# Optimization experiments

Hardware: AMD Instinct MI355X
Metric: run time of the kernel (lower is better)

Reference implementation:

```python
import jax, jax.numpy as jnp
import numpy as np

DELTA_SCALE = 0.99
DELTA_MIN = 0.01


def setup_inputs() -> dict:
    key = jax.random.key(0)
    ks = jax.random.split(key, 6)
    B, S, Dm, N = 8, 4096, 1024, 16
    x = jax.random.normal(ks[0], (B, S, Dm), dtype=jnp.float32)
    A = jax.random.normal(ks[1], (N,), dtype=jnp.float32) * 0.1 - 1.0
    W_b = jax.random.normal(ks[2], (N, Dm), dtype=jnp.float32) / np.sqrt(Dm)
    b_b = jnp.zeros((N,), dtype=jnp.float32)
    W_c = jax.random.normal(ks[3], (Dm, N), dtype=jnp.float32) / np.sqrt(N)
    b_c = jnp.zeros((Dm,), dtype=jnp.float32)
    D = jnp.ones((Dm,), dtype=jnp.float32)
    W_t = jax.random.normal(ks[4], (1, Dm), dtype=jnp.float32) / np.sqrt(Dm)
    b_t = jnp.zeros((1,), dtype=jnp.float32)
    W_o = jax.random.normal(ks[5], (Dm, Dm), dtype=jnp.float32) / np.sqrt(Dm)
    b_o = jnp.zeros((Dm,), dtype=jnp.float32)
    return {"x": x, "A": A, "W_b": W_b, "b_b": b_b, "W_c": W_c, "b_c": b_c,
            "D": D, "W_t": W_t, "b_t": b_t, "W_o": W_o, "b_o": b_o}


def _scan_combine(left, right):
    # h_t = a_t * h_{t-1} + b_t ; compose two affine maps
    a_l, u_l = left
    a_r, u_r = right
    return (a_l * a_r, a_r * u_l + u_r)


def reference(x, A, W_b, b_b, W_c, b_c, D, W_t, b_t, W_o, b_o):
    # x: [B, S, Dm]
    delta = jax.nn.sigmoid(jnp.einsum('bsd,od->bso', x, W_t) + b_t)  # [B,S,1]
    delta = delta * DELTA_SCALE + DELTA_MIN
    Bu = jnp.einsum('bsd,nd->bsn', x, W_b) + b_b                     # [B,S,N]
    A_exp = jnp.exp(A[None, None, :] * delta)                        # [B,S,N]
    # Parallel associative scan over time: h_t = A_exp_t * h_{t-1} + Bu_t
    _, h = jax.lax.associative_scan(_scan_combine, (A_exp, Bu), axis=1)
    outputs = jnp.einsum('bsn,dn->bsd', h, W_c) + b_c                # [B,S,Dm]
    y = outputs + x * D[None, None, :]
    y = jnp.einsum('bsd,od->bso', y, W_o) + b_o                      # dropout = eval identity
    return y
```

## Files before the change

### kernel.cpp

```cpp
#include <hip/hip_runtime.h>
#include <hip/hip_bf16.h>
#include <cstdint>
#include <cstddef>

#define B_SZ 8
#define S_SZ 4096
#define DM   1024
#define NS   16
#define M_SZ (B_SZ * S_SZ)

typedef __attribute__((ext_vector_type(4))) float f32x4;
typedef __attribute__((ext_vector_type(8))) short short8;
typedef __attribute__((ext_vector_type(4))) unsigned short ushort4v;
typedef __attribute__((ext_vector_type(8))) unsigned short ushort8v;

__device__ __forceinline__ unsigned short f2bf(float f) {
  unsigned u = __float_as_uint(f);
  u += 0x7fffu + ((u >> 16) & 1u);
  return (unsigned short)(u >> 16);
}

__device__ __forceinline__ short8 cvt8(f32x4 a, f32x4 b) {
  short8 r;
  r[0] = (short)f2bf(a[0]); r[1] = (short)f2bf(a[1]);
  r[2] = (short)f2bf(a[2]); r[3] = (short)f2bf(a[3]);
  r[4] = (short)f2bf(b[0]); r[5] = (short)f2bf(b[1]);
  r[6] = (short)f2bf(b[2]); r[7] = (short)f2bf(b[3]);
  return r;
}

__device__ __forceinline__ void gl_lds16(const void* g, void* l) {
  __builtin_amdgcn_global_load_lds(
      (const __attribute__((address_space(1))) void*)g,
      (__attribute__((address_space(3))) void*)l, 16, 0, 0);
}

__global__ __launch_bounds__(128) void kW(const float* __restrict__ Wb,
                                          const float* __restrict__ Wt,
                                          unsigned short* __restrict__ W16s) {
  const int col = blockIdx.x;
  const int k8 = threadIdx.x;
  f32x4 a = {0.f, 0.f, 0.f, 0.f}, b = {0.f, 0.f, 0.f, 0.f};
  if (col < 16) {
    a = *(const f32x4*)(Wb + (size_t)col * DM + k8 * 8);
    b = *(const f32x4*)(Wb + (size_t)col * DM + k8 * 8 + 4);
  } else if (col == 16) {
    a = *(const f32x4*)(Wt + k8 * 8);
    b = *(const f32x4*)(Wt + k8 * 8 + 4);
  }
  short8 v = cvt8(a, b);
  const int byteoff = (col * 2048 + k8 * 16) ^ ((col & 7) << 4);
  *(short8*)((char*)W16s + byteoff) = v;
}

__global__ __launch_bounds__(256) void k0_prep(
    const float* __restrict__ Wo, const float* __restrict__ D,
    const float* __restrict__ Wc, const float* __restrict__ bc,
    const float* __restrict__ bo, unsigned short* __restrict__ WoD16,
    unsigned short* __restrict__ Wco16, float* __restrict__ bz) {
  const int o = blockIdx.x;
  const int t = threadIdx.x;
  const float* wor = Wo + (size_t)o * DM;

  f32x4 wv = *(const f32x4*)(wor + t * 4);
  f32x4 dv = *(const f32x4*)(D + t * 4);
  ushort4v u;
#pragma unroll
  for (int i = 0; i < 4; ++i) u[i] = f2bf(wv[i] * dv[i]);
  *(ushort4v*)(WoD16 + (size_t)o * DM + t * 4) = u;

  const int n = t & 15, ds = t >> 4;
  float s = 0.f;
  const float* wod = wor + ds * 64;
  const float* wcd = Wc + (size_t)(ds * 64) * NS + n;
#pragma unroll 8
  for (int j = 0; j < 64; ++j) s += wod[j] * wcd[j * NS];

  f32x4 bcv = *(const f32x4*)(bc + t * 4);
  float pb = wv[0] * bcv[0] + wv[1] * bcv[1] + wv[2] * bcv[2] + wv[3] * bcv[3];

  __shared__ float red[16][17];
  __shared__ float redb[256];
  red[n][ds] = s;
  redb[t] = pb;
  __syncthreads();
  if (t < 16) {
    float acc = 0.f;
#pragma unroll
    for (int k = 0; k < 16; ++k) acc += red[t][k];
    Wco16[(size_t)o * 32 + t] = f2bf(acc);
    Wco16[(size_t)o * 32 + 16 + t] = 0;
  }
  if (t == 0) {
    float b = bo[o];
    for (int i = 0; i < 256; ++i) b += redb[i];
    bz[o] = b;
  }
}

__global__ __launch_bounds__(256) void k1_proj(
    const float* __restrict__ x, const float* __restrict__ A,
    const unsigned short* __restrict__ W16s,
    const float* __restrict__ bb, const float* __restrict__ bt,
    float* __restrict__ Ae, float* __restrict__ Bu,
    unsigned short* __restrict__ x16) {
  __shared__ __align__(16) char Wlds[65536];
  __shared__ float Bu_s[16][65];
  __shared__ float z_s[64];
  const int tid = threadIdx.x, lane = tid & 63, w = tid >> 6;
  const int p = lane & 15, g = lane >> 4;

#pragma unroll
  for (int i = 0; i < 16; ++i)
    gl_lds16((const char*)W16s + (w * 16 + i) * 1024 + lane * 16,
             Wlds + (w * 16 + i) * 1024);
  __syncthreads();

  const int m0 = blockIdx.x * 64;
  const int m = m0 + w * 16 + p;
  const float* xp = x + (size_t)m * DM;
  unsigned short* xo = x16 + (size_t)m * DM;
  f32x4 acc0 = {0.f, 0.f, 0.f, 0.f}, acc1 = {0.f, 0.f, 0.f, 0.f};
  const int cb0 = p * 2048;
  const int cb1 = (16 + p) * 2048;
  const int sw0 = (p & 7) << 4;

#pragma unroll 2
  for (int kk = 0; kk < 32; ++kk) {
    const int k0 = kk * 32 + g * 8;
    f32x4 xa = *(const f32x4*)(xp + k0);
    f32x4 xb = *(const f32x4*)(xp + k0 + 4);
    short8 af = cvt8(xa, xb);
    *(short8*)(xo + k0) = af;
    const int kb = kk * 64 + g * 16;
    short8 b0 = *(const short8*)(Wlds + ((cb0 + kb) ^ sw0));
    short8 b1 = *(const short8*)(Wlds + ((cb1 + kb) ^ sw0));
    acc0 = __builtin_amdgcn_mfma_f32_16x16x32_bf16(af, b0, acc0, 0, 0, 0);
    acc1 = __builtin_amdgcn_mfma_f32_16x16x32_bf16(af, b1, acc1, 0, 0, 0);
  }

  const float bbn = bb[p];
#pragma unroll
  for (int r = 0; r < 4; ++r) Bu_s[p][w * 16 + g * 4 + r] = acc0[r] + bbn;
  if (p == 0) {
#pragma unroll
    for (int r = 0; r < 4; ++r) z_s[w * 16 + g * 4 + r] = acc1[r];
  }
  __syncthreads();

  const int b_idx = m0 >> 12;
  const int s0 = m0 & (S_SZ - 1);
  const int n = tid >> 4, j0 = (tid & 15) * 4;
  const float an = A[n];
  const float bt0 = bt[0];
  size_t off = ((size_t)(b_idx * NS + n)) * S_SZ + s0 + j0;
#pragma unroll
  for (int jj = 0; jj < 4; ++jj) {
    float z = z_s[j0 + jj] + bt0;
    float delta = 1.f / (1.f + __expf(-z));
    delta = delta * 0.99f + 0.01f;
    Ae[off + jj] = __expf(an * delta);
    Bu[off + jj] = Bu_s[n][j0 + jj];
  }
}

__global__ __launch_bounds__(256) void k2a(float* __restrict__ Ae, float* __restrict__ Bu,
                                           float* __restrict__ agg_a, float* __restrict__ agg_u) {
  const int l = threadIdx.x & 63, w = threadIdx.x >> 6;
  const int cid = blockIdx.x * 4 + w;
  float* ap = Ae + (size_t)cid * 256;
  float* up = Bu + (size_t)cid * 256;
  float ca = 1.f, cu = 0.f;
#pragma unroll 1
  for (int seg = 0; seg < 4; ++seg) {
    float a = ap[seg * 64 + l], u = up[seg * 64 + l];
#pragma unroll
    for (int off = 1; off < 64; off <<= 1) {
      float aL = __shfl_up(a, off, 64);
      float uL = __shfl_up(u, off, 64);
      if (l >= off) { u = a * uL + u; a = aL * a; }
    }
    float At = ca * a, Ut = a * cu + u;
    ap[seg * 64 + l] = At;
    up[seg * 64 + l] = Ut;
    ca = __shfl(At, 63, 64);
    cu = __shfl(Ut, 63, 64);
  }
  if (l == 0) { agg_a[cid] = ca; agg_u[cid] = cu; }
}

__global__ __launch_bounds__(128) void k2b(const float* __restrict__ agg_a,
                                           const float* __restrict__ agg_u,
                                           float* __restrict__ cpre) {
  const int t = threadIdx.x;
  float cu = 0.f;
#pragma unroll
  for (int c = 0; c < 16; ++c) {
    cpre[t * 16 + c] = cu;
    cu = agg_a[t * 16 + c] * cu + agg_u[t * 16 + c];
  }
}

__global__ __launch_bounds__(256) void k2c(const float* __restrict__ Ae,
                                           const float* __restrict__ Bu,
                                           const float* __restrict__ cpre,
                                           unsigned short* __restrict__ h16) {
  const int m = blockIdx.x * 256 + threadIdx.x;
  const int b = m >> 12, s = m & 4095, c = s >> 8;
  unsigned short o[32];
#pragma unroll
  for (int n = 0; n < 16; ++n) {
    size_t idx = ((size_t)(b * 16 + n)) * 4096 + s;
    float h = Ae[idx] * cpre[(b * 16 + n) * 16 + c] + Bu[idx];
    o[n] = f2bf(h);
  }
#pragma unroll
  for (int n = 16; n < 32; ++n) o[n] = 0;
  unsigned short* dst = h16 + (size_t)m * 32;
#pragma unroll
  for (int q = 0; q < 4; ++q) *(ushort8v*)(dst + q * 8) = *(const ushort8v*)(o + q * 8);
}

__global__ __launch_bounds__(256) void k4_gemm(
    const unsigned short* __restrict__ x16, const unsigned short* __restrict__ h16,
    const unsigned short* __restrict__ WoD16, const unsigned short* __restrict__ Wco16,
    const float* __restrict__ bz, float* __restrict__ C) {
  __shared__ __align__(16) char smem[32768];
  const int tid = threadIdx.x;
  const int swz = (blockIdx.x & 7) * 256 + (blockIdx.x >> 3);
  const int by = swz >> 3;
  const int bx = swz & 7;
  const int lane = tid & 63;
  const int w = tid >> 6;
  const int wm = w >> 1, wn = w & 1;
  const int p = lane & 15, g = lane >> 4;

  f32x4 acc[4][4];
#pragma unroll
  for (int i = 0; i < 4; ++i)
#pragma unroll
    for (int j = 0; j < 4; ++j) acc[i][j] = (f32x4){0.f, 0.f, 0.f, 0.f};

  {
    short8 ah[4], bh[4];
#pragma unroll
    for (int mi = 0; mi < 4; ++mi)
      ah[mi] = *(const short8*)(h16 + (size_t)(by * 128 + wm * 64 + mi * 16 + p) * 32 + g * 8);
#pragma unroll
    for (int ni = 0; ni < 4; ++ni)
      bh[ni] = *(const short8*)(Wco16 + (size_t)(bx * 128 + wn * 64 + ni * 16 + p) * 32 + g * 8);
#pragma unroll
    for (int mi = 0; mi < 4; ++mi)
#pragma unroll
      for (int ni = 0; ni < 4; ++ni)
        acc[mi][ni] = __builtin_amdgcn_mfma_f32_16x16x32_bf16(ah[mi], bh[ni],
                                                              acc[mi][ni], 0, 0, 0);
  }

  const int chunk0 = tid;
  const int chunk1 = 256 + tid;
  const int rowA0 = chunk0 >> 2, colA0 = chunk0 & 3;
  const int rowA1 = chunk1 >> 2, colA1 = chunk1 & 3;
  const unsigned short* Abase = x16 + (size_t)(by * 128) * DM;
  const unsigned short* Bbase = WoD16 + (size_t)(bx * 128) * DM;

#define STAGE(buf, kk)                                                              \
  do {                                                                              \
    char* sb = smem + (buf) * 16384;                                                \
    const int k0_ = (kk) * 32;                                                      \
    gl_lds16(Abase + (size_t)rowA0 * DM + k0_ + colA0 * 8, sb + chunk0 * 16);       \
    gl_lds16(Abase + (size_t)rowA1 * DM + k0_ + colA1 * 8, sb + chunk1 * 16);       \
    gl_lds16(Bbase + (size_t)rowA0 * DM + k0_ + colA0 * 8, sb + 8192 + chunk0 * 16);\
    gl_lds16(Bbase + (size_t)rowA1 * DM + k0_ + colA1 * 8, sb + 8192 + chunk1 * 16);\
  } while (0)

  STAGE(0, 0);
  __syncthreads();
  int cur = 0;
#pragma unroll 1
  for (int kk = 0; kk < 32; ++kk) {
    if (kk < 31) STAGE(cur ^ 1, kk + 1);
    const char* sb = smem + cur * 16384;
    short8 af[4], bfr[4];
#pragma unroll
    for (int mi = 0; mi < 4; ++mi)
      af[mi] = *(const short8*)(sb + (wm * 64 + mi * 16 + p) * 64 + g * 16);
#pragma unroll
    for (int ni = 0; ni < 4; ++ni)
      bfr[ni] = *(const short8*)(sb + 8192 + (wn * 64 + ni * 16 + p) * 64 + g * 16);
#pragma unroll
    for (int mi = 0; mi < 4; ++mi)
#pragma unroll
      for (int ni = 0; ni < 4; ++ni)
        acc[mi][ni] = __builtin_amdgcn_mfma_f32_16x16x32_bf16(af[mi], bfr[ni],
                                                              acc[mi][ni], 0, 0, 0);
    __syncthreads();
    cur ^= 1;
  }
#undef STAGE

#pragma unroll
  for (int ni = 0; ni < 4; ++ni) {
    const int c0 = bx * 128 + wn * 64 + ni * 16 + p;
    const float bzv = bz[c0];
#pragma unroll
    for (int mi = 0; mi < 4; ++mi) {
      const int r0 = by * 128 + wm * 64 + mi * 16 + g * 4;
#pragma unroll
      for (int r = 0; r < 4; ++r)
        C[(size_t)(r0 + r) * DM + c0] = acc[mi][ni][r] + bzv;
    }
  }
}

extern "C" void kernel_launch(void* const* d_in, const int* in_sizes, int n_in,
                              void* d_out, int out_size, void* d_ws, size_t ws_size,
                              hipStream_t stream) {
  const float* x  = (const float*)d_in[0];
  const float* A  = (const float*)d_in[1];
  const float* Wb = (const float*)d_in[2];
  const float* bb = (const float*)d_in[3];
  const float* Wc = (const float*)d_in[4];
  const float* bc = (const float*)d_in[5];
  const float* D  = (const float*)d_in[6];
  const float* Wt = (const float*)d_in[7];
  const float* bt = (const float*)d_in[8];
  const float* Wo = (const float*)d_in[9];
  const float* bo = (const float*)d_in[10];
  float* out = (float*)d_out;

  char* ws = (char*)d_ws;
  float* Ae            = (float*)(ws);
  float* Bu            = (float*)(ws + (2u << 20));
  unsigned short* h16  = (unsigned short*)(ws + (4u << 20));
  unsigned short* WoD16= (unsigned short*)(ws + (6u << 20));
  unsigned short* Wco16= (unsigned short*)(ws + (8u << 20));
  float* bz            = (float*)(ws + (8u << 20) + (64u << 10));
  unsigned short* W16s = (unsigned short*)(ws + (8u << 20) + (68u << 10));
  float* agg_a         = (float*)(ws + (8u << 20) + (132u << 10));
  float* agg_u         = (float*)(ws + (8u << 20) + (140u << 10));
  float* cpre          = (float*)(ws + (8u << 20) + (148u << 10));
  unsigned short* x16  = (unsigned short*)(ws + (9u << 20));

  kW<<<32, 128, 0, stream>>>(Wb, Wt, W16s);
  k0_prep<<<1024, 256, 0, stream>>>(Wo, D, Wc, bc, bo, WoD16, Wco16, bz);
  k1_proj<<<512, 256, 0, stream>>>(x, A, W16s, bb, bt, Ae, Bu, x16);
  k2a<<<512, 256, 0, stream>>>(Ae, Bu, agg_a, agg_u);
  k2b<<<1, 128, 0, stream>>>(agg_a, agg_u, cpre);
  k2c<<<128, 256, 0, stream>>>(Ae, Bu, cpre, h16);
  k4_gemm<<<2048, 256, 0, stream>>>(x16, h16, WoD16, Wco16, bz, out);
}
```

Baseline: 366.2 us.

## Enlarge GEMM tiles with swizzled LDS pipeline and fold small kernels together

```diff
diff --git a/kernel.cpp b/kernel.cpp
--- a/kernel.cpp
+++ b/kernel.cpp
@@ -35,31 +35,32 @@
       (__attribute__((address_space(3))) void*)l, 16, 0, 0);
 }
 
-__global__ __launch_bounds__(128) void kW(const float* __restrict__ Wb,
-                                          const float* __restrict__ Wt,
-                                          unsigned short* __restrict__ W16s) {
-  const int col = blockIdx.x;
-  const int k8 = threadIdx.x;
-  f32x4 a = {0.f, 0.f, 0.f, 0.f}, b = {0.f, 0.f, 0.f, 0.f};
-  if (col < 16) {
-    a = *(const f32x4*)(Wb + (size_t)col * DM + k8 * 8);
-    b = *(const f32x4*)(Wb + (size_t)col * DM + k8 * 8 + 4);
-  } else if (col == 16) {
-    a = *(const f32x4*)(Wt + k8 * 8);
-    b = *(const f32x4*)(Wt + k8 * 8 + 4);
-  }
-  short8 v = cvt8(a, b);
-  const int byteoff = (col * 2048 + k8 * 16) ^ ((col & 7) << 4);
-  *(short8*)((char*)W16s + byteoff) = v;
-}
+#define SB() __builtin_amdgcn_sched_barrier(0)
+__device__ __forceinline__ void bar() { SB(); __builtin_amdgcn_s_barrier(); SB(); }
+#define VMW4 asm volatile("s_waitcnt vmcnt(4)" ::: "memory")
+#define VMW0 asm volatile("s_waitcnt vmcnt(0)" ::: "memory")
+#define VMNOP (void)0
 
 __global__ __launch_bounds__(256) void k0_prep(
     const float* __restrict__ Wo, const float* __restrict__ D,
     const float* __restrict__ Wc, const float* __restrict__ bc,
     const float* __restrict__ bo, unsigned short* __restrict__ WoD16,
-    unsigned short* __restrict__ Wco16, float* __restrict__ bz) {
+    unsigned short* __restrict__ Wco16, float* __restrict__ bz,
+    const float* __restrict__ Wb, const float* __restrict__ Wt,
+    unsigned short* __restrict__ W16s) {
+  const int t = threadIdx.x;
+  if (blockIdx.x >= 1024) {
+    const int col = blockIdx.x - 1024;
+    f32x4 a = {0.f, 0.f, 0.f, 0.f};
+    if (col < 16)       a = *(const f32x4*)(Wb + (size_t)col * DM + t * 4);
+    else if (col == 16) a = *(const f32x4*)(Wt + t * 4);
+    ushort4v u;
+#pragma unroll
+    for (int i = 0; i < 4; ++i) u[i] = f2bf(a[i]);
+    *(ushort4v*)((char*)W16s + ((col * 2048 + t * 8) ^ ((col & 7) << 4))) = u;
+    return;
+  }
   const int o = blockIdx.x;
-  const int t = threadIdx.x;
   const float* wor = Wo + (size_t)o * DM;
 
   f32x4 wv = *(const f32x4*)(wor + t * 4);
@@ -91,10 +92,11 @@
     Wco16[(size_t)o * 32 + t] = f2bf(acc);
     Wco16[(size_t)o * 32 + 16 + t] = 0;
   }
-  if (t == 0) {
-    float b = bo[o];
-    for (int i = 0; i < 256; ++i) b += redb[i];
-    bz[o] = b;
+  if (t < 64) {
+    float s4 = redb[t] + redb[t + 64] + redb[t + 128] + redb[t + 192];
+#pragma unroll
+    for (int mb = 1; mb < 64; mb <<= 1) s4 += __shfl_xor(s4, mb, 64);
+    if (t == 0) bz[o] = bo[o] + s4;
   }
 }
 
@@ -189,29 +191,27 @@
   if (l == 0) { agg_a[cid] = ca; agg_u[cid] = cu; }
 }
 
-__global__ __launch_bounds__(128) void k2b(const float* __restrict__ agg_a,
-                                           const float* __restrict__ agg_u,
-                                           float* __restrict__ cpre) {
-  const int t = threadIdx.x;
-  float cu = 0.f;
-#pragma unroll
-  for (int c = 0; c < 16; ++c) {
-    cpre[t * 16 + c] = cu;
-    cu = agg_a[t * 16 + c] * cu + agg_u[t * 16 + c];
-  }
-}
-
 __global__ __launch_bounds__(256) void k2c(const float* __restrict__ Ae,
                                            const float* __restrict__ Bu,
-                                           const float* __restrict__ cpre,
+                                           const float* __restrict__ agg_a,
+                                           const float* __restrict__ agg_u,
                                            unsigned short* __restrict__ h16) {
-  const int m = blockIdx.x * 256 + threadIdx.x;
+  const int t = threadIdx.x;
+  const int m = blockIdx.x * 256 + t;
   const int b = m >> 12, s = m & 4095, c = s >> 8;
+  __shared__ float cp_s[16];
+  if (t < 16) {
+    float cu = 0.f;
+    const int base = (b * 16 + t) * 16;
+    for (int c2 = 0; c2 < c; ++c2) cu = agg_a[base + c2] * cu + agg_u[base + c2];
+    cp_s[t] = cu;
+  }
+  __syncthreads();
   unsigned short o[32];
 #pragma unroll
   for (int n = 0; n < 16; ++n) {
     size_t idx = ((size_t)(b * 16 + n)) * 4096 + s;
-    float h = Ae[idx] * cpre[(b * 16 + n) * 16 + c] + Bu[idx];
+    float h = Ae[idx] * cp_s[n] + Bu[idx];
     o[n] = f2bf(h);
   }
 #pragma unroll
@@ -221,94 +221,130 @@
   for (int q = 0; q < 4; ++q) *(ushort8v*)(dst + q * 8) = *(const ushort8v*)(o + q * 8);
 }
 
-__global__ __launch_bounds__(256) void k4_gemm(
+__global__ __launch_bounds__(512, 2) void k4_gemm(
     const unsigned short* __restrict__ x16, const unsigned short* __restrict__ h16,
     const unsigned short* __restrict__ WoD16, const unsigned short* __restrict__ Wco16,
     const float* __restrict__ bz, float* __restrict__ C) {
-  __shared__ __align__(16) char smem[32768];
+  __shared__ __align__(16) char smem[131072];
   const int tid = threadIdx.x;
-  const int swz = (blockIdx.x & 7) * 256 + (blockIdx.x >> 3);
-  const int by = swz >> 3;
-  const int bx = swz & 7;
+  const int swzid = (blockIdx.x & 7) * 64 + (blockIdx.x >> 3);
+  const int by = swzid >> 2;
+  const int bx = swzid & 3;
   const int lane = tid & 63;
   const int w = tid >> 6;
-  const int wm = w >> 1, wn = w & 1;
+  const int wm = w >> 2, wn = w & 3;
   const int p = lane & 15, g = lane >> 4;
-
-  f32x4 acc[4][4];
-#pragma unroll
-  for (int i = 0; i < 4; ++i)
+  const int cbsw = (g * 16) ^ (((p >> 1) & 3) << 4);
+
+  f32x4 acc[8][4];
+#pragma unroll
+  for (int i = 0; i < 8; ++i)
 #pragma unroll
     for (int j = 0; j < 4; ++j) acc[i][j] = (f32x4){0.f, 0.f, 0.f, 0.f};
 
   {
-    short8 ah[4], bh[4];
-#pragma unroll
-    for (int mi = 0; mi < 4; ++mi)
-      ah[mi] = *(const short8*)(h16 + (size_t)(by * 128 + wm * 64 + mi * 16 + p) * 32 + g * 8);
+    short8 ah[8], bh[4];
+#pragma unroll
+    for (int mi = 0; mi < 8; ++mi)
+      ah[mi] = *(const short8*)(h16 + (size_t)(by * 256 + wm * 128 + mi * 16 + p) * 32 + g * 8);
 #pragma unroll
     for (int ni = 0; ni < 4; ++ni)
-      bh[ni] = *(const short8*)(Wco16 + (size_t)(bx * 128 + wn * 64 + ni * 16 + p) * 32 + g * 8);
-#pragma unroll
-    for (int mi = 0; mi < 4; ++mi)
+      bh[ni] = *(const short8*)(Wco16 + (size_t)(bx * 256 + wn * 64 + ni * 16 + p) * 32 + g * 8);
+#pragma unroll
+    for (int mi = 0; mi < 8; ++mi)
 #pragma unroll
       for (int ni = 0; ni < 4; ++ni)
         acc[mi][ni] = __builtin_amdgcn_mfma_f32_16x16x32_bf16(ah[mi], bh[ni],
                                                               acc[mi][ni], 0, 0, 0);
   }
-
-  const int chunk0 = tid;
-  const int chunk1 = 256 + tid;
-  const int rowA0 = chunk0 >> 2, colA0 = chunk0 & 3;
-  const int rowA1 = chunk1 >> 2, colA1 = chunk1 & 3;
-  const unsigned short* Abase = x16 + (size_t)(by * 128) * DM;
-  const unsigned short* Bbase = WoD16 + (size_t)(bx * 128) * DM;
-
-#define STAGE(buf, kk)                                                              \
-  do {                                                                              \
-    char* sb = smem + (buf) * 16384;                                                \
-    const int k0_ = (kk) * 32;                                                      \
-    gl_lds16(Abase + (size_t)rowA0 * DM + k0_ + colA0 * 8, sb + chunk0 * 16);       \
-    gl_lds16(Abase + (size_t)rowA1 * DM + k0_ + colA1 * 8, sb + chunk1 * 16);       \
-    gl_lds16(Bbase + (size_t)rowA0 * DM + k0_ + colA0 * 8, sb + 8192 + chunk0 * 16);\
-    gl_lds16(Bbase + (size_t)rowA1 * DM + k0_ + colA1 * 8, sb + 8192 + chunk1 * 16);\
+  SB();
+
+  const char* Ag = (const char*)(x16 + (size_t)(by * 256) * DM);
+  const char* Bg = (const char*)(WoD16 + (size_t)(bx * 256) * DM);
+  const int L0 = tid * 16, L1 = 8192 + tid * 16;
+  const int r0 = L0 >> 6, r1 = L1 >> 6;
+  const size_t ga0 = (size_t)r0 * 2048 + ((L0 & 63) ^ (((r0 >> 1) & 3) << 4));
+  const size_t ga1 = (size_t)r1 * 2048 + ((L1 & 63) ^ (((r1 >> 1) & 3) << 4));
+
+#define STG_A(d, kh, t_)                                                        \
+  do { const int ko_ = (t_) * 128 + (kh) * 64;                                  \
+    gl_lds16(Ag + ga0 + ko_, smem + (d) * 32768 + (kh) * 16384 + L0);           \
+    gl_lds16(Ag + ga1 + ko_, smem + (d) * 32768 + (kh) * 16384 + L1); } while (0)
+#define STG_B(d, kh, t_)                                                        \
+  do { const int ko_ = (t_) * 128 + (kh) * 64;                                  \
+    gl_lds16(Bg + ga0 + ko_, smem + 65536 + (d) * 32768 + (kh) * 16384 + L0);   \
+    gl_lds16(Bg + ga1 + ko_, smem + 65536 + (d) * 32768 + (kh) * 16384 + L1); } while (0)
+
+#define PHASE(d, kh, mh, STAGE_STMT, VMSTMT)                                    \
+  do {                                                                          \
+    const char* ab_ = smem + (d) * 32768 + (kh) * 16384;                        \
+    const char* bb_ = smem + 65536 + (d) * 32768 + (kh) * 16384;                \
+    short8 af0 = *(const short8*)(ab_ + (wm * 128 + ((mh) * 4 + 0) * 16 + p) * 64 + cbsw); \
+    short8 af1 = *(const short8*)(ab_ + (wm * 128 + ((mh) * 4 + 1) * 16 + p) * 64 + cbsw); \
+    short8 af2 = *(const short8*)(ab_ + (wm * 128 + ((mh) * 4 + 2) * 16 + p) * 64 + cbsw); \
+    short8 af3 = *(const short8*)(ab_ + (wm * 128 + ((mh) * 4 + 3) * 16 + p) * 64 + cbsw); \
+    short8 bf0 = *(const short8*)(bb_ + (wn * 64 + 0 * 16 + p) * 64 + cbsw);    \
+    short8 bf1 = *(const short8*)(bb_ + (wn * 64 + 1 * 16 + p) * 64 + cbsw);    \
+    short8 bf2 = *(const short8*)(bb_ + (wn * 64 + 2 * 16 + p) * 64 + cbsw);    \
+    short8 bf3 = *(const short8*)(bb_ + (wn * 64 + 3 * 16 + p) * 64 + cbsw);    \
+    STAGE_STMT;                                                                 \
+    bar();                                                                      \
+    __builtin_amdgcn_s_setprio(1);                                              \
+    acc[(mh)*4+0][0] = __builtin_amdgcn_mfma_f32_16x16x32_bf16(af0, bf0, acc[(mh)*4+0][0], 0, 0, 0); \
+    acc[(mh)*4+0][1] = __builtin_amdgcn_mfma_f32_16x16x32_bf16(af0, bf1, acc[(mh)*4+0][1], 0, 0, 0); \
+    acc[(mh)*4+0][2] = __builtin_amdgcn_mfma_f32_16x16x32_bf16(af0, bf2, acc[(mh)*4+0][2], 0, 0, 0); \
+    acc[(mh)*4+0][3] = __builtin_amdgcn_mfma_f32_16x16x32_bf16(af0, bf3, acc[(mh)*4+0][3], 0, 0, 0); \
+    acc[(mh)*4+1][0] = __builtin_amdgcn_mfma_f32_16x16x32_bf16(af1, bf0, acc[(mh)*4+1][0], 0, 0, 0); \
+    acc[(mh)*4+1][1] = __builtin_amdgcn_mfma_f32_16x16x32_bf16(af1, bf1, acc[(mh)*4+1][1], 0, 0, 0); \
+    acc[(mh)*4+1][2] = __builtin_amdgcn_mfma_f32_16x16x32_bf16(af1, bf2, acc[(mh)*4+1][2], 0, 0, 0); \
+    acc[(mh)*4+1][3] = __builtin_amdgcn_mfma_f32_16x16x32_bf16(af1, bf3, acc[(mh)*4+1][3], 0, 0, 0); \
+    acc[(mh)*4+2][0] = __builtin_amdgcn_mfma_f32_16x16x32_bf16(af2, bf0, acc[(mh)*4+2][0], 0, 0, 0); \
+    acc[(mh)*4+2][1] = __builtin_amdgcn_mfma_f32_16x16x32_bf16(af2, bf1, acc[(mh)*4+2][1], 0, 0, 0); \
+    acc[(mh)*4+2][2] = __builtin_amdgcn_mfma_f32_16x16x32_bf16(af2, bf2, acc[(mh)*4+2][2], 0, 0, 0); \
+    acc[(mh)*4+2][3] = __builtin_amdgcn_mfma_f32_16x16x32_bf16(af2, bf3, acc[(mh)*4+2][3], 0, 0, 0); \
+    acc[(mh)*4+3][0] = __builtin_amdgcn_mfma_f32_16x16x32_bf16(af3, bf0, acc[(mh)*4+3][0], 0, 0, 0); \
+    acc[(mh)*4+3][1] = __builtin_amdgcn_mfma_f32_16x16x32_bf16(af3, bf1, acc[(mh)*4+3][1], 0, 0, 0); \
+    acc[(mh)*4+3][2] = __builtin_amdgcn_mfma_f32_16x16x32_bf16(af3, bf2, acc[(mh)*4+3][2], 0, 0, 0); \
+    acc[(mh)*4+3][3] = __builtin_amdgcn_mfma_f32_16x16x32_bf16(af3, bf3, acc[(mh)*4+3][3], 0, 0, 0); \
+    __builtin_amdgcn_s_setprio(0);                                              \
+    VMSTMT;                                                                     \
+    bar();                                                                      \
   } while (0)
 
-  STAGE(0, 0);
-  __syncthreads();
-  int cur = 0;
+  STG_A(0, 0, 0); STG_B(0, 0, 0); STG_A(0, 1, 0); STG_B(0, 1, 0);
+  STG_A(1, 0, 1); STG_B(1, 0, 1);
+  VMW4;
+  bar();
+
 #pragma unroll 1
-  for (int kk = 0; kk < 32; ++kk) {
-    if (kk < 31) STAGE(cur ^ 1, kk + 1);
-    const char* sb = smem + cur * 16384;
-    short8 af[4], bfr[4];
-#pragma unroll
-    for (int mi = 0; mi < 4; ++mi)
-      af[mi] = *(const short8*)(sb + (wm * 64 + mi * 16 + p) * 64 + g * 16);
-#pragma unroll
-    for (int ni = 0; ni < 4; ++ni)
-      bfr[ni] = *(const short8*)(sb + 8192 + (wn * 64 + ni * 16 + p) * 64 + g * 16);
-#pragma unroll
-    for (int mi = 0; mi < 4; ++mi)
-#pragma unroll
-      for (int ni = 0; ni < 4; ++ni)
-        acc[mi][ni] = __builtin_amdgcn_mfma_f32_16x16x32_bf16(af[mi], bfr[ni],
-                                                              acc[mi][ni], 0, 0, 0);
-    __syncthreads();
-    cur ^= 1;
-  }
-#undef STAGE
+  for (int i = 0; i < 8; ++i) {
+    const int t1 = 2 * i + 1;
+    const int t2 = (2 * i + 2 > 15) ? 15 : 2 * i + 2;
+    const int t3 = (2 * i + 3 > 15) ? 15 : 2 * i + 3;
+    PHASE(0, 0, 0, STG_A(1, 1, t1), VMNOP);
+    PHASE(0, 0, 1, STG_B(1, 1, t1), VMNOP);
+    PHASE(0, 1, 0, STG_A(0, 0, t2), VMNOP);
+    PHASE(0, 1, 1, STG_B(0, 0, t2), VMW4);
+    PHASE(1, 0, 0, STG_A(0, 1, t2), VMNOP);
+    PHASE(1, 0, 1, STG_B(0, 1, t2), VMNOP);
+    PHASE(1, 1, 0, STG_A(1, 0, t3), VMNOP);
+    PHASE(1, 1, 1, STG_B(1, 0, t3), VMW4);
+  }
+  VMW0;
+#undef PHASE
+#undef STG_A
+#undef STG_B
 
 #pragma unroll
   for (int ni = 0; ni < 4; ++ni) {
-    const int c0 = bx * 128 + wn * 64 + ni * 16 + p;
+    const int c0 = bx * 256 + wn * 64 + ni * 16 + p;
     const float bzv = bz[c0];
 #pragma unroll
-    for (int mi = 0; mi < 4; ++mi) {
-      const int r0 = by * 128 + wm * 64 + mi * 16 + g * 4;
+    for (int mi = 0; mi < 8; ++mi) {
+      const int r0w = by * 256 + wm * 128 + mi * 16 + g * 4;
 #pragma unroll
       for (int r = 0; r < 4; ++r)
-        C[(size_t)(r0 + r) * DM + c0] = acc[mi][ni][r] + bzv;
+        C[(size_t)(r0w + r) * DM + c0] = acc[mi][ni][r] + bzv;
     }
   }
 }
@@ -339,14 +375,11 @@
   unsigned short* W16s = (unsigned short*)(ws + (8u << 20) + (68u << 10));
   float* agg_a         = (float*)(ws + (8u << 20) + (132u << 10));
   float* agg_u         = (float*)(ws + (8u << 20) + (140u << 10));
-  float* cpre          = (float*)(ws + (8u << 20) + (148u << 10));
   unsigned short* x16  = (unsigned short*)(ws + (9u << 20));
 
-  kW<<<32, 128, 0, stream>>>(Wb, Wt, W16s);
-  k0_prep<<<1024, 256, 0, stream>>>(Wo, D, Wc, bc, bo, WoD16, Wco16, bz);
+  k0_prep<<<1056, 256, 0, stream>>>(Wo, D, Wc, bc, bo, WoD16, Wco16, bz, Wb, Wt, W16s);
   k1_proj<<<512, 256, 0, stream>>>(x, A, W16s, bb, bt, Ae, Bu, x16);
   k2a<<<512, 256, 0, stream>>>(Ae, Bu, agg_a, agg_u);
-  k2b<<<1, 128, 0, stream>>>(agg_a, agg_u, cpre);
-  k2c<<<128, 256, 0, stream>>>(Ae, Bu, cpre, h16);
-  k4_gemm<<<2048, 256, 0, stream>>>(x16, h16, WoD16, Wco16, bz, out);
-}
+  k2c<<<128, 256, 0, stream>>>(Ae, Bu, agg_a, agg_u, h16);
+  k4_gemm<<<512, 512, 0, stream>>>(x16, h16, WoD16, Wco16, bz, out);
+}
```

Measured after the change: 356.0 us. 2.8% less time.
